# Optimization experiments

Measured on AMD Instinct MI355X. Metric: run time of the kernel, lower is better.

## Reference

```python
import jax, jax.numpy as jnp
import numpy as np

B, S, L = 8, 2048, 8
H, NH = 768, 12
DH = H // NH
NUM_REL = 100
LN_EPS = 1e-5


def setup_inputs() -> dict:
    key = jax.random.key(0)
    ks = jax.random.split(key, 16)
    inp = {
        'text_embeddings': jax.random.normal(ks[0], (B, S, H), dtype=jnp.float32),
        # values in [-1, 64); -1 marks 'no leaf' and is masked out
        'graph_structure': jax.random.randint(ks[1], (B, S, L), -1, 64, dtype=jnp.int64),
        'relation_ids': jax.random.randint(ks[2], (B, S, L), 0, NUM_REL, dtype=jnp.int64),
        'rel_table': jax.random.normal(ks[3], (NUM_REL, H), dtype=jnp.float32),
        'Wq': jax.random.normal(ks[4], (H, H), dtype=jnp.float32) / np.sqrt(H),
        'bq': jnp.zeros((H,), dtype=jnp.float32),
        'Wk': jax.random.normal(ks[5], (H, H), dtype=jnp.float32) / np.sqrt(H),
        'bk': jnp.zeros((H,), dtype=jnp.float32),
        'Wv': jax.random.normal(ks[6], (H, H), dtype=jnp.float32) / np.sqrt(H),
        'bv': jnp.zeros((H,), dtype=jnp.float32),
        'Wo': jax.random.normal(ks[7], (H, H), dtype=jnp.float32) / np.sqrt(H),
        'bo': jnp.zeros((H,), dtype=jnp.float32),
        'gamma': jnp.ones((H,), dtype=jnp.float32),
        'beta': jnp.zeros((H,), dtype=jnp.float32),
    }
    return inp


def reference(text_embeddings, graph_structure, relation_ids, rel_table,
              Wq, bq, Wk, bk, Wv, bv, Wo, bo, gamma, beta):
    b, s, h = text_embeddings.shape
    l = relation_ids.shape[2]
    # embedding gather (clamp -1 -> 0, masked later)
    rel_emb = rel_table[jnp.clip(relation_ids, 0, None)]  # [B,S,L,H]
    # projections; query has length-1 per root token
    q = (text_embeddings @ Wq + bq).reshape(b, s, NH, DH)          # [B,S,N,D]
    k = (rel_emb @ Wk + bk).reshape(b, s, l, NH, DH)               # [B,S,L,N,D]
    v = (rel_emb @ Wv + bv).reshape(b, s, l, NH, DH)
    scores = jnp.einsum('bsnd,bslnd->bsnl', q, k) / np.sqrt(DH)    # [B,S,N,L]
    mask = (graph_structure != -1)[:, :, None, :]                  # [B,S,1,L]
    scores = jnp.where(mask, scores, jnp.float32(-10000.0))
    probs = jax.nn.softmax(scores, axis=-1)                        # [B,S,N,L]
    ctx = jnp.einsum('bsnl,bslnd->bsnd', probs, v).reshape(b, s, h)
    out = ctx @ Wo + bo
    x = text_embeddings + out
    mu = jnp.mean(x, axis=-1, keepdims=True)
    var = jnp.mean(jnp.square(x - mu), axis=-1, keepdims=True)
    return (x - mu) * jax.lax.rsqrt(var + LN_EPS) * gamma + beta
```

## Files before the change

### kernel.cpp

```cpp
#include <hip/hip_runtime.h>
#include <hip/hip_bf16.h>

#define H 768
#define NH 12
#define DH 64
#define LL 8
#define NTOK 16384
#define NREL 100
#define NRELP 128
#define PADW 72

typedef __attribute__((ext_vector_type(8))) short short8;
typedef __attribute__((ext_vector_type(4))) float f32x4;

__device__ __forceinline__ float bf2f(ushort u) {
  union { unsigned int i; float f; } v; v.i = ((unsigned int)u) << 16; return v.f;
}
__device__ __forceinline__ float bflo(unsigned int u) {
  union { unsigned int i; float f; } v; v.i = u << 16; return v.f;
}
__device__ __forceinline__ float bfhi(unsigned int u) {
  union { unsigned int i; float f; } v; v.i = u & 0xffff0000u; return v.f;
}
__device__ __forceinline__ ushort f2bf(float f) {
  union { float f; unsigned int i; } v; v.f = f;
  unsigned int x = v.i;
  return (ushort)((x + 0x7fffu + ((x >> 16) & 1u)) >> 16);
}
__device__ __forceinline__ unsigned int cvt_pk_bf16(float lo, float hi) {
  unsigned int r;
  asm("v_cvt_pk_bf16_f32 %0, %1, %2" : "=v"(r) : "v"(lo), "v"(hi));
  return r;
}

__global__ __launch_bounds__(256) void prep_kernel(
    const float* __restrict__ s0, ushort* __restrict__ d0,
    const float* __restrict__ s1, ushort* __restrict__ d1,
    const float* __restrict__ s2, ushort* __restrict__ d2,
    const float* __restrict__ s3, ushort* __restrict__ d3,
    const float* __restrict__ rel, ushort* __restrict__ RelB) {
  if (blockIdx.z == 4) {
    int b = blockIdx.y * 24 + blockIdx.x;
    if (b < 96) {
      int i = (b * 256 + threadIdx.x) * 4;
      int row = i / H;
      ushort4 o = {0, 0, 0, 0};
      if (row < NREL) {
        float4 v = *(const float4*)(rel + i);
        o.x = f2bf(v.x); o.y = f2bf(v.y); o.z = f2bf(v.z); o.w = f2bf(v.w);
      }
      *(ushort4*)(RelB + i) = o;
    }
    return;
  }
  const float* src; ushort* dst;
  switch (blockIdx.z) {
    case 0:  src = s0; dst = d0; break;
    case 1:  src = s1; dst = d1; break;
    case 2:  src = s2; dst = d2; break;
    default: src = s3; dst = d3; break;
  }
  __shared__ float tile[32][33];
  int bx = blockIdx.x * 32, by = blockIdx.y * 32;
  int tx = threadIdx.x & 31, ty = threadIdx.x >> 5;
  #pragma unroll
  for (int i = 0; i < 32; i += 8)
    tile[ty + i][tx] = src[(size_t)(by + ty + i) * H + bx + tx];
  __syncthreads();
  #pragma unroll
  for (int i = 0; i < 32; i += 8)
    dst[(size_t)(bx + ty + i) * H + by + tx] = f2bf(tile[tx][ty + i]);
}

__device__ __forceinline__ void gload_lds16(const void* g, void* l) {
  __builtin_amdgcn_global_load_lds(
      (const __attribute__((address_space(1))) unsigned int*)g,
      (__attribute__((address_space(3))) unsigned int*)l, 16, 0, 0);
}

#define BM 64
#define BN 128
#define BK 64
#define ATILE (BM * BK)
#define BTILE (BN * BK)

#define GEMM_COMPUTE(cb)                                                       \
  _Pragma("unroll")                                                            \
  for (int kk = 0; kk < 2; ++kk) {                                             \
    const int sw = (((kk << 2) | lk) ^ (lr & 7)) * 8;                          \
    short8 af[2], bfr[4];                                                      \
    _Pragma("unroll")                                                          \
    for (int m = 0; m < 2; ++m)                                                \
      af[m] = *(const short8*)(As + (cb) * ATILE + (wr * 32 + m * 16 + lr) * BK + sw); \
    _Pragma("unroll")                                                          \
    for (int n = 0; n < 4; ++n)                                                \
      bfr[n] = *(const short8*)(Bs + (cb) * BTILE + (wc * 64 + n * 16 + lr) * BK + sw); \
    _Pragma("unroll")                                                          \
    for (int m = 0; m < 2; ++m)                                                \
      _Pragma("unroll")                                                        \
      for (int n = 0; n < 4; ++n)                                              \
        acc[m][n] = __builtin_amdgcn_mfma_f32_16x16x32_bf16(af[m], bfr[n],     \
                                                            acc[m][n], 0, 0, 0);\
  }

#define GEMM_EPILOGUE()                                                        \
  _Pragma("unroll")                                                            \
  for (int m = 0; m < 2; ++m) {                                                \
    _Pragma("unroll")                                                          \
    for (int n = 0; n < 4; ++n) {                                              \
      int col = col0 + wc * 64 + n * 16 + lr;                                  \
      float b = bias[col];                                                     \
      _Pragma("unroll")                                                        \
      for (int j = 0; j < 4; ++j) {                                            \
        int row = row0 + wr * 32 + m * 16 + lk * 4 + j;                        \
        C[(size_t)row * N + col] = f2bf(acc[m][n][j] + b);                     \
      }                                                                        \
    }                                                                          \
  }

__device__ __forceinline__ void gemm_body(
    ushort* As, ushort* Bs,
    const ushort* __restrict__ A,
    const ushort* __restrict__ Bt,
    const float* __restrict__ bias,
    ushort* __restrict__ C,
    int M, int N, int K, int bx, int by) {
  const int tid = threadIdx.x;
  const int row0 = by * BM;
  const int col0 = bx * BN;
  const int wave = tid >> 6;
  const int lane = tid & 63;
  const int wr = wave >> 1, wc = wave & 1;
  const int lr = lane & 15, lk = lane >> 4;
  f32x4 acc[2][4];
  #pragma unroll
  for (int m = 0; m < 2; ++m)
    #pragma unroll
    for (int n = 0; n < 4; ++n) acc[m][n] = (f32x4)(0.f);

  const int nt = K / BK;
  #pragma unroll
  for (int i = 0; i < 2; ++i) {
    int c = tid + i * 256; int r = c >> 3, s = c & 7; int gsx = s ^ (r & 7);
    gload_lds16(A + (size_t)(row0 + r) * K + gsx * 8, (char*)As + c * 16);
  }
  #pragma unroll
  for (int i = 0; i < 4; ++i) {
    int c = tid + i * 256; int r = c >> 3, s = c & 7; int gsx = s ^ (r & 7);
    gload_lds16(Bt + (size_t)(col0 + r) * K + gsx * 8, (char*)Bs + c * 16);
  }
  __syncthreads();
  int cb = 0;
  for (int t = 0; t < nt; ++t) {
    if (t + 1 < nt) {
      int k1 = (t + 1) * BK;
      #pragma unroll
      for (int i = 0; i < 2; ++i) {
        int c = tid + i * 256; int r = c >> 3, s = c & 7; int gsx = s ^ (r & 7);
        gload_lds16(A + (size_t)(row0 + r) * K + k1 + gsx * 8,
                    (char*)As + (cb ^ 1) * (ATILE * 2) + c * 16);
      }
      #pragma unroll
      for (int i = 0; i < 4; ++i) {
        int c = tid + i * 256; int r = c >> 3, s = c & 7; int gsx = s ^ (r & 7);
        gload_lds16(Bt + (size_t)(col0 + r) * K + k1 + gsx * 8,
                    (char*)Bs + (cb ^ 1) * (BTILE * 2) + c * 16);
      }
    }
    GEMM_COMPUTE(cb)
    __syncthreads();
    cb ^= 1;
  }
  GEMM_EPILOGUE()
}

__device__ __forceinline__ void gemm_body_a32(
    ushort* As, ushort* Bs,
    const float* __restrict__ A32,
    const ushort* __restrict__ Bt,
    const float* __restrict__ bias,
    ushort* __restrict__ C,
    int M, int N, int K, int bx, int by) {
  const int tid = threadIdx.x;
  const int row0 = by * BM;
  const int col0 = bx * BN;
  const int wave = tid >> 6;
  const int lane = tid & 63;
  const int wr = wave >> 1, wc = wave & 1;
  const int lr = lane & 15, lk = lane >> 4;
  f32x4 acc[2][4];
  #pragma unroll
  for (int m = 0; m < 2; ++m)
    #pragma unroll
    for (int n = 0; n < 4; ++n) acc[m][n] = (f32x4)(0.f);

  const int nt = K / BK;
  #pragma unroll
  for (int i = 0; i < 4; ++i) {
    int c = tid + i * 256; int r = c >> 3, s = c & 7; int gsx = s ^ (r & 7);
    gload_lds16(Bt + (size_t)(col0 + r) * K + gsx * 8, (char*)Bs + c * 16);
  }
  #pragma unroll
  for (int i = 0; i < 2; ++i) {
    int c = tid + i * 256; int r = c >> 3, s = c & 7; int gsx = s ^ (r & 7);
    const float* src = A32 + (size_t)(row0 + r) * K + gsx * 8;
    float4 f0 = *(const float4*)(src);
    float4 f1 = *(const float4*)(src + 4);
    uint4 w;
    w.x = cvt_pk_bf16(f0.x, f0.y);
    w.y = cvt_pk_bf16(f0.z, f0.w);
    w.z = cvt_pk_bf16(f1.x, f1.y);
    w.w = cvt_pk_bf16(f1.z, f1.w);
    *(uint4*)((char*)As + c * 16) = w;
  }
  __syncthreads();
  int cb = 0;
  for (int t = 0; t < nt; ++t) {
    float4 fa0, fa1, fb0, fb1;
    if (t + 1 < nt) {
      int k1 = (t + 1) * BK;
      #pragma unroll
      for (int i = 0; i < 4; ++i) {
        int c = tid + i * 256; int r = c >> 3, s = c & 7; int gsx = s ^ (r & 7);
        gload_lds16(Bt + (size_t)(col0 + r) * K + k1 + gsx * 8,
                    (char*)Bs + (cb ^ 1) * (BTILE * 2) + c * 16);
      }
      {
        int c = tid;            int r = c >> 3, s = c & 7; int gsx = s ^ (r & 7);
        const float* src = A32 + (size_t)(row0 + r) * K + k1 + gsx * 8;
        fa0 = *(const float4*)(src); fa1 = *(const float4*)(src + 4);
      }
      {
        int c = tid + 256;      int r = c >> 3, s = c & 7; int gsx = s ^ (r & 7);
        const float* src = A32 + (size_t)(row0 + r) * K + k1 + gsx * 8;
        fb0 = *(const float4*)(src); fb1 = *(const float4*)(src + 4);
      }
    }
    GEMM_COMPUTE(cb)
    if (t + 1 < nt) {
      uint4 w;
      w.x = cvt_pk_bf16(fa0.x, fa0.y); w.y = cvt_pk_bf16(fa0.z, fa0.w);
      w.z = cvt_pk_bf16(fa1.x, fa1.y); w.w = cvt_pk_bf16(fa1.z, fa1.w);
      *(uint4*)((char*)As + (cb ^ 1) * (ATILE * 2) + tid * 16) = w;
      w.x = cvt_pk_bf16(fb0.x, fb0.y); w.y = cvt_pk_bf16(fb0.z, fb0.w);
      w.z = cvt_pk_bf16(fb1.x, fb1.y); w.w = cvt_pk_bf16(fb1.z, fb1.w);
      *(uint4*)((char*)As + (cb ^ 1) * (ATILE * 2) + (tid + 256) * 16) = w;
    }
    __syncthreads();
    cb ^= 1;
  }
  GEMM_EPILOGUE()
}

__global__ __launch_bounds__(256, 3) void gemm_q_kv_kernel(
    const float* __restrict__ X, const ushort* __restrict__ WqT,
    const float* __restrict__ bq, ushort* __restrict__ Qbf,
    const ushort* __restrict__ RelB,
    const ushort* __restrict__ WkT, const float* __restrict__ bk, ushort* __restrict__ Ktab,
    const ushort* __restrict__ WvT, const float* __restrict__ bv, ushort* __restrict__ Vtab) {
  __shared__ ushort As[2 * ATILE];
  __shared__ ushort Bs[2 * BTILE];
  int lin = blockIdx.x;
  if (lin < 24) {
    if (lin < 12)
      gemm_body(As, Bs, RelB, WkT, bk, Ktab, NRELP, H, H, lin % 6, lin / 6);
    else {
      int l = lin - 12;
      gemm_body(As, Bs, RelB, WvT, bv, Vtab, NRELP, H, H, l % 6, l / 6);
    }
    return;
  }
  int l2 = lin - 24;
  int wg = (l2 & 7) * 192 + (l2 >> 3);
  gemm_body_a32(As, Bs, X, WqT, bq, Qbf, NTOK, H, H, wg % 6, wg / 6);
}

__global__ __launch_bounds__(256, 3) void gemm_bt_kernel(
    const ushort* __restrict__ A, const ushort* __restrict__ Bt,
    const float* __restrict__ bias, ushort* __restrict__ C,
    int M, int N, int K) {
  __shared__ ushort As[2 * ATILE];
  __shared__ ushort Bs[2 * BTILE];
  int lin = blockIdx.y * gridDim.x + blockIdx.x;
  int q = (gridDim.x * gridDim.y) >> 3;
  int wg = (lin & 7) * q + (lin >> 3);
  gemm_body(As, Bs, A, Bt, bias, C, M, N, K, wg % gridDim.x, wg / gridDim.x);
}

__global__ __launch_bounds__(256) void attn3_kernel(
    const ushort* __restrict__ Q,
    const ushort* __restrict__ Ktab,
    const ushort* __restrict__ Vtab,
    const int* __restrict__ graph,
    const int* __restrict__ relid,
    ushort* __restrict__ Ctx) {
  __shared__ __align__(16) ushort Ks[NREL * PADW];
  __shared__ __align__(16) ushort Vs[NREL * PADW];
  const int tid = threadIdx.x;
  const int head = blockIdx.y;
  const int t = blockIdx.x * 256 + tid;

  #pragma unroll
  for (int i = 0; i < 4; ++i) {
    int c = tid + i * 256;
    if (c < NREL * 9) {
      int row = c / 9, slot = c - row * 9;
      int gsx = (slot < 8) ? slot * 8 : 0;
      const size_t src = (size_t)row * H + head * DH + gsx;
      gload_lds16(Ktab + src, (char*)Ks + (size_t)c * 16);
      gload_lds16(Vtab + src, (char*)Vs + (size_t)c * 16);
    }
  }

  const uint4* qp = (const uint4*)(Q + (size_t)t * H + head * DH);
  uint4 qw[8];
  #pragma unroll
  for (int j = 0; j < 8; ++j) qw[j] = qp[j];
  const int4* gp = (const int4*)(graph + (size_t)t * LL);
  const int4* rp = (const int4*)(relid + (size_t)t * LL);
  int4 ga = gp[0], gb = gp[1];
  int4 ra = rp[0], rb = rp[1];
  int gs[8] = {ga.x, ga.y, ga.z, ga.w, gb.x, gb.y, gb.z, gb.w};
  int rid[8] = {ra.x, ra.y, ra.z, ra.w, rb.x, rb.y, rb.z, rb.w};
  int koff[8];
  #pragma unroll
  for (int l = 0; l < 8; ++l) {
    int r = rid[l] < 0 ? 0 : rid[l];
    koff[l] = r * (PADW * 2);
  }

  __syncthreads();

  float s[8];
  #pragma unroll
  for (int l = 0; l < 8; ++l) s[l] = 0.f;
  #pragma unroll
  for (int j = 0; j < 8; ++j) {
    float qf[8];
    qf[0] = bflo(qw[j].x); qf[1] = bfhi(qw[j].x);
    qf[2] = bflo(qw[j].y); qf[3] = bfhi(qw[j].y);
    qf[4] = bflo(qw[j].z); qf[5] = bfhi(qw[j].z);
    qf[6] = bflo(qw[j].w); qf[7] = bfhi(qw[j].w);
    #pragma unroll
    for (int l = 0; l < 8; ++l) {
      uint4 kw = *(const uint4*)((const char*)Ks + koff[l] + j * 16);
      s[l] += qf[0] * bflo(kw.x) + qf[1] * bfhi(kw.x)
            + qf[2] * bflo(kw.y) + qf[3] * bfhi(kw.y)
            + qf[4] * bflo(kw.z) + qf[5] * bfhi(kw.z)
            + qf[6] * bflo(kw.w) + qf[7] * bfhi(kw.w);
    }
  }

  #pragma unroll
  for (int l = 0; l < 8; ++l)
    s[l] = (gs[l] != -1) ? s[l] * 0.125f : -10000.0f;
  float mx = s[0];
  #pragma unroll
  for (int l = 1; l < 8; ++l) mx = fmaxf(mx, s[l]);
  float p[8], den = 0.f;
  #pragma unroll
  for (int l = 0; l < 8; ++l) { p[l] = __expf(s[l] - mx); den += p[l]; }
  float inv = 1.f / den;
  #pragma unroll
  for (int l = 0; l < 8; ++l) p[l] *= inv;

  ushort* cp = Ctx + (size_t)t * H + head * DH;
  #pragma unroll
  for (int j = 0; j < 8; ++j) {
    float a[8];
    #pragma unroll
    for (int d = 0; d < 8; ++d) a[d] = 0.f;
    #pragma unroll
    for (int l = 0; l < 8; ++l) {
      uint4 vw = *(const uint4*)((const char*)Vs + koff[l] + j * 16);
      a[0] += p[l] * bflo(vw.x); a[1] += p[l] * bfhi(vw.x);
      a[2] += p[l] * bflo(vw.y); a[3] += p[l] * bfhi(vw.y);
      a[4] += p[l] * bflo(vw.z); a[5] += p[l] * bfhi(vw.z);
      a[6] += p[l] * bflo(vw.w); a[7] += p[l] * bfhi(vw.w);
    }
    short8 o;
    #pragma unroll
    for (int d = 0; d < 8; ++d) o[d] = (short)f2bf(a[d]);
    *(short8*)(cp + j * 8) = o;
  }
}

__global__ __launch_bounds__(192) void ln_kernel(
    const float* __restrict__ text, const ushort* __restrict__ op,
    const float* __restrict__ gamma, const float* __restrict__ beta,
    float* __restrict__ out) {
  int t = blockIdx.x;
  int c0 = threadIdx.x * 4;
  float4 tv = *(const float4*)(text + (size_t)t * H + c0);
  ushort4 ov = *(const ushort4*)(op + (size_t)t * H + c0);
  float x0 = tv.x + bf2f(ov.x), x1 = tv.y + bf2f(ov.y);
  float x2 = tv.z + bf2f(ov.z), x3 = tv.w + bf2f(ov.w);
  float s = x0 + x1 + x2 + x3;
  float s2 = x0 * x0 + x1 * x1 + x2 * x2 + x3 * x3;
  #pragma unroll
  for (int off = 32; off > 0; off >>= 1) {
    s  += __shfl_xor(s, off, 64);
    s2 += __shfl_xor(s2, off, 64);
  }
  __shared__ float red[2][3];
  int wave = threadIdx.x >> 6, lane = threadIdx.x & 63;
  if (lane == 0) { red[0][wave] = s; red[1][wave] = s2; }
  __syncthreads();
  s  = red[0][0] + red[0][1] + red[0][2];
  s2 = red[1][0] + red[1][1] + red[1][2];
  float mu = s * (1.f / H);
  float var = s2 * (1.f / H) - mu * mu;
  float rs = rsqrtf(var + 1e-5f);
  float4 g4 = *(const float4*)(gamma + c0);
  float4 b4 = *(const float4*)(beta + c0);
  float4 o4;
  o4.x = (x0 - mu) * rs * g4.x + b4.x;
  o4.y = (x1 - mu) * rs * g4.y + b4.y;
  o4.z = (x2 - mu) * rs * g4.z + b4.z;
  o4.w = (x3 - mu) * rs * g4.w + b4.w;
  *(float4*)(out + (size_t)t * H + c0) = o4;
}

extern "C" void kernel_launch(void* const* d_in, const int* in_sizes, int n_in,
                              void* d_out, int out_size, void* d_ws, size_t ws_size,
                              hipStream_t stream) {
  const float* text      = (const float*)d_in[0];
  const int*   graph     = (const int*)d_in[1];
  const int*   relid     = (const int*)d_in[2];
  const float* rel_table = (const float*)d_in[3];
  const float* Wq = (const float*)d_in[4];  const float* bq = (const float*)d_in[5];
  const float* Wk = (const float*)d_in[6];  const float* bk = (const float*)d_in[7];
  const float* Wv = (const float*)d_in[8];  const float* bv = (const float*)d_in[9];
  const float* Wo = (const float*)d_in[10]; const float* bo = (const float*)d_in[11];
  const float* gamma = (const float*)d_in[12];
  const float* beta  = (const float*)d_in[13];
  float* out = (float*)d_out;
  char* ws = (char*)d_ws;

  const size_t TOKH = (size_t)NTOK * H;
  size_t off = 0;
  ushort* Ctx  = (ushort*)(ws + off); off += TOKH * 2;
  ushort* Qbf  = (ushort*)(ws + off); off += TOKH * 2;
  ushort* WqT  = (ushort*)(ws + off); off += (size_t)H * H * 2;
  ushort* WoT  = (ushort*)(ws + off); off += (size_t)H * H * 2;
  ushort* WkT  = (ushort*)(ws + off); off += (size_t)H * H * 2;
  ushort* WvT  = (ushort*)(ws + off); off += (size_t)H * H * 2;
  ushort* RelB = (ushort*)(ws + off); off += (size_t)NRELP * H * 2;
  ushort* Ktab = (ushort*)(ws + off); off += (size_t)NRELP * H * 2;
  ushort* Vtab = (ushort*)(ws + off); off += (size_t)NRELP * H * 2;

  prep_kernel<<<dim3(24, 24, 5), 256, 0, stream>>>(
      Wq, WqT, Wo, WoT, Wk, WkT, Wv, WvT, rel_table, RelB);
  gemm_q_kv_kernel<<<24 + 1536, 256, 0, stream>>>(
      text, WqT, bq, Qbf, RelB, WkT, bk, Ktab, WvT, bv, Vtab);
  dim3 ga(NTOK / 256, NH);
  attn3_kernel<<<ga, 256, 0, stream>>>(Qbf, Ktab, Vtab, graph, relid, Ctx);
  dim3 g1(H / BN, NTOK / BM);
  gemm_bt_kernel<<<g1, 256, 0, stream>>>(Ctx, WoT, bo, Qbf, NTOK, H, H);
  ln_kernel<<<NTOK, 192, 0, stream>>>(text, Qbf, gamma, beta, out);
}
```

Baseline: 121.8 us.

## Load GEMM A fragments directly to registers, drop A shared-memory staging

Both GEMM bodies now skip staging the A tile in LDS. Each lane loads its MFMA A fragments straight from global memory into registers and prefetches the next k-tile into a second register set, while B stays double-buffered in LDS. In the fp32-A path the bf16 conversion now runs in registers just before compute. This removes LDS traffic and shared memory for A, so launch bounds rise from 3 to 4 blocks per SM. The cost is that the two column waves now fetch the same A rows redundantly from global memory, with less coalescing, and register pressure goes up.

```diff
diff --git a/kernel.cpp b/kernel.cpp
--- a/kernel.cpp
+++ b/kernel.cpp
@@ -81,17 +81,21 @@
 #define BM 64
 #define BN 128
 #define BK 64
-#define ATILE (BM * BK)
 #define BTILE (BN * BK)
 
-#define GEMM_COMPUTE(cb)                                                       \
+#define STAGE_B(k0, buf)                                                       \
+  _Pragma("unroll")                                                            \
+  for (int i = 0; i < 4; ++i) {                                                \
+    int c = tid + i * 256; int r = c >> 3, sgl = c & 7; int g = sgl ^ (r & 7); \
+    gload_lds16(Bt + (size_t)(col0 + r) * K + (k0) + g * 8,                    \
+                (char*)Bs + (buf) * (BTILE * 2) + c * 16);                     \
+  }
+
+#define GEMM_COMPUTE(cb, AF)                                                   \
   _Pragma("unroll")                                                            \
   for (int kk = 0; kk < 2; ++kk) {                                             \
     const int sw = (((kk << 2) | lk) ^ (lr & 7)) * 8;                          \
-    short8 af[2], bfr[4];                                                      \
-    _Pragma("unroll")                                                          \
-    for (int m = 0; m < 2; ++m)                                                \
-      af[m] = *(const short8*)(As + (cb) * ATILE + (wr * 32 + m * 16 + lr) * BK + sw); \
+    short8 bfr[4];                                                             \
     _Pragma("unroll")                                                          \
     for (int n = 0; n < 4; ++n)                                                \
       bfr[n] = *(const short8*)(Bs + (cb) * BTILE + (wc * 64 + n * 16 + lr) * BK + sw); \
@@ -99,7 +103,7 @@
     for (int m = 0; m < 2; ++m)                                                \
       _Pragma("unroll")                                                        \
       for (int n = 0; n < 4; ++n)                                              \
-        acc[m][n] = __builtin_amdgcn_mfma_f32_16x16x32_bf16(af[m], bfr[n],     \
+        acc[m][n] = __builtin_amdgcn_mfma_f32_16x16x32_bf16(AF[m][kk], bfr[n], \
                                                             acc[m][n], 0, 0, 0);\
   }
 
@@ -119,7 +123,7 @@
   }
 
 __device__ __forceinline__ void gemm_body(
-    ushort* As, ushort* Bs,
+    ushort* Bs,
     const ushort* __restrict__ A,
     const ushort* __restrict__ Bt,
     const float* __restrict__ bias,
@@ -139,43 +143,40 @@
     for (int n = 0; n < 4; ++n) acc[m][n] = (f32x4)(0.f);
 
   const int nt = K / BK;
-  #pragma unroll
-  for (int i = 0; i < 2; ++i) {
-    int c = tid + i * 256; int r = c >> 3, s = c & 7; int gsx = s ^ (r & 7);
-    gload_lds16(A + (size_t)(row0 + r) * K + gsx * 8, (char*)As + c * 16);
-  }
-  #pragma unroll
-  for (int i = 0; i < 4; ++i) {
-    int c = tid + i * 256; int r = c >> 3, s = c & 7; int gsx = s ^ (r & 7);
-    gload_lds16(Bt + (size_t)(col0 + r) * K + gsx * 8, (char*)Bs + c * 16);
-  }
+  const ushort* arow0 = A + (size_t)(row0 + wr * 32 + lr) * K + lk * 8;
+  const ushort* arow1 = arow0 + (size_t)16 * K;
+
+  STAGE_B(0, 0)
+  short8 curA[2][2];
+  curA[0][0] = *(const short8*)(arow0);
+  curA[0][1] = *(const short8*)(arow0 + 32);
+  curA[1][0] = *(const short8*)(arow1);
+  curA[1][1] = *(const short8*)(arow1 + 32);
   __syncthreads();
   int cb = 0;
   for (int t = 0; t < nt; ++t) {
+    short8 nxtA[2][2];
     if (t + 1 < nt) {
       int k1 = (t + 1) * BK;
-      #pragma unroll
-      for (int i = 0; i < 2; ++i) {
-        int c = tid + i * 256; int r = c >> 3, s = c & 7; int gsx = s ^ (r & 7);
-        gload_lds16(A + (size_t)(row0 + r) * K + k1 + gsx * 8,
-                    (char*)As + (cb ^ 1) * (ATILE * 2) + c * 16);
-      }
-      #pragma unroll
-      for (int i = 0; i < 4; ++i) {
-        int c = tid + i * 256; int r = c >> 3, s = c & 7; int gsx = s ^ (r & 7);
-        gload_lds16(Bt + (size_t)(col0 + r) * K + k1 + gsx * 8,
-                    (char*)Bs + (cb ^ 1) * (BTILE * 2) + c * 16);
-      }
-    }
-    GEMM_COMPUTE(cb)
+      STAGE_B(k1, cb ^ 1)
+      nxtA[0][0] = *(const short8*)(arow0 + k1);
+      nxtA[0][1] = *(const short8*)(arow0 + k1 + 32);
+      nxtA[1][0] = *(const short8*)(arow1 + k1);
+      nxtA[1][1] = *(const short8*)(arow1 + k1 + 32);
+    }
+    GEMM_COMPUTE(cb, curA)
     __syncthreads();
     cb ^= 1;
+    if (t + 1 < nt) {
+      curA[0][0] = nxtA[0][0]; curA[0][1] = nxtA[0][1];
+      curA[1][0] = nxtA[1][0]; curA[1][1] = nxtA[1][1];
+    }
   }
   GEMM_EPILOGUE()
 }
 
 __device__ __forceinline__ void gemm_body_a32(
-    ushort* As, ushort* Bs,
+    ushort* Bs,
     const float* __restrict__ A32,
     const ushort* __restrict__ Bt,
     const float* __restrict__ bias,
@@ -195,96 +196,92 @@
     for (int n = 0; n < 4; ++n) acc[m][n] = (f32x4)(0.f);
 
   const int nt = K / BK;
-  #pragma unroll
-  for (int i = 0; i < 4; ++i) {
-    int c = tid + i * 256; int r = c >> 3, s = c & 7; int gsx = s ^ (r & 7);
-    gload_lds16(Bt + (size_t)(col0 + r) * K + gsx * 8, (char*)Bs + c * 16);
-  }
-  #pragma unroll
-  for (int i = 0; i < 2; ++i) {
-    int c = tid + i * 256; int r = c >> 3, s = c & 7; int gsx = s ^ (r & 7);
-    const float* src = A32 + (size_t)(row0 + r) * K + gsx * 8;
-    float4 f0 = *(const float4*)(src);
-    float4 f1 = *(const float4*)(src + 4);
-    uint4 w;
-    w.x = cvt_pk_bf16(f0.x, f0.y);
-    w.y = cvt_pk_bf16(f0.z, f0.w);
-    w.z = cvt_pk_bf16(f1.x, f1.y);
-    w.w = cvt_pk_bf16(f1.z, f1.w);
-    *(uint4*)((char*)As + c * 16) = w;
+  const float* arow0 = A32 + (size_t)(row0 + wr * 32 + lr) * K + lk * 8;
+  const float* arow1 = arow0 + (size_t)16 * K;
+
+  STAGE_B(0, 0)
+  float4 curF[2][2][2];
+  #pragma unroll
+  for (int kk = 0; kk < 2; ++kk) {
+    curF[0][kk][0] = *(const float4*)(arow0 + kk * 32);
+    curF[0][kk][1] = *(const float4*)(arow0 + kk * 32 + 4);
+    curF[1][kk][0] = *(const float4*)(arow1 + kk * 32);
+    curF[1][kk][1] = *(const float4*)(arow1 + kk * 32 + 4);
   }
   __syncthreads();
   int cb = 0;
   for (int t = 0; t < nt; ++t) {
-    float4 fa0, fa1, fb0, fb1;
+    float4 nxtF[2][2][2];
     if (t + 1 < nt) {
       int k1 = (t + 1) * BK;
+      STAGE_B(k1, cb ^ 1)
       #pragma unroll
-      for (int i = 0; i < 4; ++i) {
-        int c = tid + i * 256; int r = c >> 3, s = c & 7; int gsx = s ^ (r & 7);
-        gload_lds16(Bt + (size_t)(col0 + r) * K + k1 + gsx * 8,
-                    (char*)Bs + (cb ^ 1) * (BTILE * 2) + c * 16);
+      for (int kk = 0; kk < 2; ++kk) {
+        nxtF[0][kk][0] = *(const float4*)(arow0 + k1 + kk * 32);
+        nxtF[0][kk][1] = *(const float4*)(arow0 + k1 + kk * 32 + 4);
+        nxtF[1][kk][0] = *(const float4*)(arow1 + k1 + kk * 32);
+        nxtF[1][kk][1] = *(const float4*)(arow1 + k1 + kk * 32 + 4);
       }
-      {
-        int c = tid;            int r = c >> 3, s = c & 7; int gsx = s ^ (r & 7);
-        const float* src = A32 + (size_t)(row0 + r) * K + k1 + gsx * 8;
-        fa0 = *(const float4*)(src); fa1 = *(const float4*)(src + 4);
+    }
+    short8 curA[2][2];
+    #pragma unroll
+    for (int m = 0; m < 2; ++m)
+      #pragma unroll
+      for (int kk = 0; kk < 2; ++kk) {
+        union { uint4 u; short8 s8; } cv;
+        cv.u.x = cvt_pk_bf16(curF[m][kk][0].x, curF[m][kk][0].y);
+        cv.u.y = cvt_pk_bf16(curF[m][kk][0].z, curF[m][kk][0].w);
+        cv.u.z = cvt_pk_bf16(curF[m][kk][1].x, curF[m][kk][1].y);
+        cv.u.w = cvt_pk_bf16(curF[m][kk][1].z, curF[m][kk][1].w);
+        curA[m][kk] = cv.s8;
       }
-      {
-        int c = tid + 256;      int r = c >> 3, s = c & 7; int gsx = s ^ (r & 7);
-        const float* src = A32 + (size_t)(row0 + r) * K + k1 + gsx * 8;
-        fb0 = *(const float4*)(src); fb1 = *(const float4*)(src + 4);
-      }
-    }
-    GEMM_COMPUTE(cb)
-    if (t + 1 < nt) {
-      uint4 w;
-      w.x = cvt_pk_bf16(fa0.x, fa0.y); w.y = cvt_pk_bf16(fa0.z, fa0.w);
-      w.z = cvt_pk_bf16(fa1.x, fa1.y); w.w = cvt_pk_bf16(fa1.z, fa1.w);
-      *(uint4*)((char*)As + (cb ^ 1) * (ATILE * 2) + tid * 16) = w;
-      w.x = cvt_pk_bf16(fb0.x, fb0.y); w.y = cvt_pk_bf16(fb0.z, fb0.w);
-      w.z = cvt_pk_bf16(fb1.x, fb1.y); w.w = cvt_pk_bf16(fb1.z, fb1.w);
-      *(uint4*)((char*)As + (cb ^ 1) * (ATILE * 2) + (tid + 256) * 16) = w;
-    }
+    GEMM_COMPUTE(cb, curA)
     __syncthreads();
     cb ^= 1;
+    if (t + 1 < nt) {
+      #pragma unroll
+      for (int m = 0; m < 2; ++m)
+        #pragma unroll
+        for (int kk = 0; kk < 2; ++kk) {
+          curF[m][kk][0] = nxtF[m][kk][0];
+          curF[m][kk][1] = nxtF[m][kk][1];
+        }
+    }
   }
   GEMM_EPILOGUE()
 }
 
-__global__ __launch_bounds__(256, 3) void gemm_q_kv_kernel(
+__global__ __launch_bounds__(256, 4) void gemm_q_kv_kernel(
     const float* __restrict__ X, const ushort* __restrict__ WqT,
     const float* __restrict__ bq, ushort* __restrict__ Qbf,
     const ushort* __restrict__ RelB,
     const ushort* __restrict__ WkT, const float* __restrict__ bk, ushort* __restrict__ Ktab,
     const ushort* __restrict__ WvT, const float* __restrict__ bv, ushort* __restrict__ Vtab) {
-  __shared__ ushort As[2 * ATILE];
   __shared__ ushort Bs[2 * BTILE];
   int lin = blockIdx.x;
   if (lin < 24) {
     if (lin < 12)
-      gemm_body(As, Bs, RelB, WkT, bk, Ktab, NRELP, H, H, lin % 6, lin / 6);
+      gemm_body(Bs, RelB, WkT, bk, Ktab, NRELP, H, H, lin % 6, lin / 6);
     else {
       int l = lin - 12;
-      gemm_body(As, Bs, RelB, WvT, bv, Vtab, NRELP, H, H, l % 6, l / 6);
+      gemm_body(Bs, RelB, WvT, bv, Vtab, NRELP, H, H, l % 6, l / 6);
     }
     return;
   }
   int l2 = lin - 24;
   int wg = (l2 & 7) * 192 + (l2 >> 3);
-  gemm_body_a32(As, Bs, X, WqT, bq, Qbf, NTOK, H, H, wg % 6, wg / 6);
-}
-
-__global__ __launch_bounds__(256, 3) void gemm_bt_kernel(
+  gemm_body_a32(Bs, X, WqT, bq, Qbf, NTOK, H, H, wg % 6, wg / 6);
+}
+
+__global__ __launch_bounds__(256, 4) void gemm_bt_kernel(
     const ushort* __restrict__ A, const ushort* __restrict__ Bt,
     const float* __restrict__ bias, ushort* __restrict__ C,
     int M, int N, int K) {
-  __shared__ ushort As[2 * ATILE];
   __shared__ ushort Bs[2 * BTILE];
   int lin = blockIdx.y * gridDim.x + blockIdx.x;
   int q = (gridDim.x * gridDim.y) >> 3;
   int wg = (lin & 7) * q + (lin >> 3);
-  gemm_body(As, Bs, A, Bt, bias, C, M, N, K, wg % gridDim.x, wg / gridDim.x);
+  gemm_body(Bs, A, Bt, bias, C, M, N, K, wg % gridDim.x, wg / gridDim.x);
 }
 
 __global__ __launch_bounds__(256) void attn3_kernel(
```

Result: slower. 179.3 us (+47.2%).
